# Kernel tuning notes

Measured on AMD Instinct MI355X. Metric: run time of the kernel, lower is better.

## Reference

```python
import jax, jax.numpy as jnp
import numpy as np

H = 512  # hidden_size


def _highway_lstm(x, lengths, Wi, bi, Ws, bs):
    B, T, D = x.shape
    # Precompute all input projections in one big GEMM: [B, T, 6H]
    pi = jnp.einsum('btd,kd->btk', x, Wi) + bi
    mask = jnp.arange(T)[None, :] < lengths[:, None]  # [B, T]

    def step(carry, inp):
        h, c = carry
        pi_t, m = inp                      # pi_t: [B, 6H], m: [B]
        ps = h @ Ws.T + bs                 # [B, 5H]
        i = jax.nn.sigmoid(pi_t[:, 0*H:1*H] + ps[:, 0*H:1*H])
        f = jax.nn.sigmoid(pi_t[:, 1*H:2*H] + ps[:, 1*H:2*H])
        g = jnp.tanh(pi_t[:, 2*H:3*H] + ps[:, 2*H:3*H])
        o = jax.nn.sigmoid(pi_t[:, 3*H:4*H] + ps[:, 3*H:4*H])
        c_new = i * g + f * c
        out = o * jnp.tanh(c_new)
        # highway gate blends LSTM output with linear input projection
        r = jax.nn.sigmoid(pi_t[:, 4*H:5*H] + ps[:, 4*H:5*H])
        out = r * out + (1.0 - r) * pi_t[:, 5*H:6*H]
        m2 = m[:, None]
        h_new = jnp.where(m2, out, h)      # hold state past sequence end
        c_new = jnp.where(m2, c_new, c)
        y = jnp.where(m2, out, jnp.zeros_like(out))  # packed-seq padding = 0
        return (h_new, c_new), y

    h0 = jnp.zeros((B, H), x.dtype)
    c0 = jnp.zeros((B, H), x.dtype)
    (hT, cT), ys = jax.lax.scan(step, (h0, c0),
                                (jnp.swapaxes(pi, 0, 1), mask.T))
    return jnp.swapaxes(ys, 0, 1), hT, cT  # outputs [B,T,H], final (h, c)


def setup_inputs() -> dict:
    key = jax.random.key(0)
    ks = jax.random.split(key, 4)
    B, T, D = 32, 512, 512
    x = jax.random.normal(ks[0], (B, T, D), dtype=jnp.float32)
    lengths = jax.random.randint(ks[1], (B,), 1, T + 1, dtype=jnp.int32)
    Wi = jax.random.normal(ks[2], (6 * H, D), dtype=jnp.float32) * 0.05
    bi = jnp.zeros((6 * H,), dtype=jnp.float32)
    Ws = jax.random.normal(ks[3], (5 * H, H), dtype=jnp.float32) * 0.05
    bs = jnp.zeros((5 * H,), dtype=jnp.float32)
    return {"x": x, "lengths": lengths, "Wi": Wi, "bi": bi, "Ws": Ws, "bs": bs}


def reference(x, lengths, Wi, bi, Ws, bs):
    return _highway_lstm(x, lengths, Wi, bi, Ws, bs)
```

## Files before the change

### kernel.cpp

```cpp
#include <hip/hip_runtime.h>
#include <stdint.h>

typedef __attribute__((ext_vector_type(8))) short short8;
typedef __attribute__((ext_vector_type(4))) float f32x4;
typedef unsigned long long u64;

constexpr int cB = 32, cT = 512, cD = 512, cH = 512;
constexpr int cKI = 6 * cH;
constexpr int NWG = 32;
constexpr int THR = 320;
constexpr int HP  = 520;
constexpr int RNG = 3;
constexpr int PIP = 40;
constexpr int FPAD = 16;
constexpr int GK = 24, GN = 128;

constexpr int OFF_PIL  = 32 * HP * 2;
constexpr int OFF_PS   = OFF_PIL + RNG * 6 * 16 * PIP * 2;
constexpr int OFF_C    = OFF_PS + 5 * 16 * 36 * 4;
constexpr int OFF_BS   = OFF_C + 512 * 4;
constexpr int OFF_LEN  = OFF_BS + 80 * 4;
constexpr int OFF_MISC = OFF_LEN + 32 * 4;
constexpr int SMEM_SZ  = OFF_MISC + 16;

__device__ __forceinline__ float bf2f(unsigned short u) {
  union { unsigned int i; float f; } x; x.i = ((unsigned int)u) << 16; return x.f;
}
__device__ __forceinline__ unsigned short f2bf(float f) {
  union { float f; unsigned int i; } x; x.f = f;
  return (unsigned short)((x.i + 0x7fffu + ((x.i >> 16) & 1u)) >> 16);
}
__device__ __forceinline__ float sigm(float v) { return 1.0f / (1.0f + __expf(-v)); }
__device__ __forceinline__ float tanh_f(float v) { return 2.0f / (1.0f + __expf(-2.0f * v)) - 1.0f; }

__global__ __launch_bounds__(THR, 1) void fused_lstm(
    const float* __restrict__ x,
    const float* __restrict__ Wi,
    const float* __restrict__ bi,
    const float* __restrict__ Ws,
    const float* __restrict__ bs,
    const int* __restrict__ lengths,
    unsigned short* __restrict__ pi,
    unsigned short* __restrict__ hbuf,
    int* __restrict__ flags,
    float* __restrict__ out)
{
  __shared__ __align__(16) unsigned char smem[SMEM_SZ];
  const int tid = threadIdx.x;
  const int lane = tid & 63;
  const int w = tid >> 6;

  if (blockIdx.x >= NWG) {
    const int gb = (int)blockIdx.x - NWG;
    const int kb = gb % GK, nbk = gb / GK;
    const int k0 = kb * 128, n0 = nbk * 128;
    unsigned short* Ai = (unsigned short*)smem;
    unsigned short* Bi = (unsigned short*)(smem + 10240);
    const int wm = w & 1, wn = w >> 1;

    f32x4 acc[4][4];
    #pragma unroll
    for (int i = 0; i < 4; i++)
      #pragma unroll
      for (int j = 0; j < 4; j++) acc[i][j] = (f32x4){0.f, 0.f, 0.f, 0.f};

    for (int kk = 0; kk < cD; kk += 32) {
      __syncthreads();
      for (int idx = tid; idx < 1024; idx += THR) {
        int r = idx >> 3, ch = idx & 7;
        int na = n0 + r, bb = na & 31, tt = na >> 5;
        float4 va = *(const float4*)(x + ((size_t)bb * cT + tt) * cD + kk + ch * 4);
        ushort4 pa; pa.x = f2bf(va.x); pa.y = f2bf(va.y); pa.z = f2bf(va.z); pa.w = f2bf(va.w);
        *(ushort4*)(Ai + r * PIP + ch * 4) = pa;
        float4 vb = *(const float4*)(Wi + (size_t)(k0 + r) * cD + kk + ch * 4);
        ushort4 pb; pb.x = f2bf(vb.x); pb.y = f2bf(vb.y); pb.z = f2bf(vb.z); pb.w = f2bf(vb.w);
        *(ushort4*)(Bi + r * PIP + ch * 4) = pb;
      }
      __syncthreads();
      if (w < 4) {
        short8 af[4], bfr[4];
        const int q = lane >> 4;
        #pragma unroll
        for (int mi = 0; mi < 4; mi++)
          af[mi] = *(const short8*)(Ai + (wm * 64 + mi * 16 + (lane & 15)) * PIP + q * 8);
        #pragma unroll
        for (int ni = 0; ni < 4; ni++)
          bfr[ni] = *(const short8*)(Bi + (wn * 64 + ni * 16 + (lane & 15)) * PIP + q * 8);
        #pragma unroll
        for (int mi = 0; mi < 4; mi++)
          #pragma unroll
          for (int ni = 0; ni < 4; ni++)
            acc[mi][ni] = __builtin_amdgcn_mfma_f32_16x16x32_bf16(af[mi], bfr[ni], acc[mi][ni], 0, 0, 0);
      }
    }
    if (w < 4) {
      #pragma unroll
      for (int ni = 0; ni < 4; ni++) {
        int kl = wn * 64 + ni * 16 + (lane & 15);
        float bv = bi[k0 + kl];
        #pragma unroll
        for (int mi = 0; mi < 4; mi++) {
          int nl = wm * 64 + mi * 16 + (lane >> 4) * 4;
          int nb = n0 + nl;
          int b0 = nb & 31, tt = nb >> 5;
          f32x4 a = acc[mi][ni];
          unsigned short v0 = f2bf(a.x + bv), v1 = f2bf(a.y + bv);
          unsigned short v2 = f2bf(a.z + bv), v3 = f2bf(a.w + bv);
          u64 pk = (u64)v0 | ((u64)v1 << 16) | ((u64)v2 << 32) | ((u64)v3 << 48);
          __hip_atomic_store((u64*)(pi + ((size_t)tt * cKI + k0 + kl) * cB + b0), pk,
                             __ATOMIC_RELAXED, __HIP_MEMORY_SCOPE_AGENT);
        }
      }
    }
    __syncthreads();
    if (tid == 0) {
      __hip_atomic_fetch_add(flags + 512 + nbk, 1, __ATOMIC_RELAXED, __HIP_MEMORY_SCOPE_AGENT);
      __hip_atomic_fetch_add(flags + 640, 1, __ATOMIC_RELAXED, __HIP_MEMORY_SCOPE_AGENT);
    }
    return;
  }

  unsigned short* h_lds  = (unsigned short*)smem;
  unsigned short* piL    = (unsigned short*)(smem + OFF_PIL);
  float* ps_lds          = (float*)(smem + OFF_PS);
  float* c_lds           = (float*)(smem + OFF_C);
  float* bs_lds          = (float*)(smem + OFF_BS);
  int*   len_lds         = (int*)(smem + OFF_LEN);
  int*   s_tr_p          = (int*)(smem + OFF_MISC);
  int*   s_all_p         = s_tr_p + 1;

  const int wg = blockIdx.x;
  const int ci0 = wg * 16;
  const int mc = lane & 15;
  const int kq = lane >> 4;

  short8 bfrag[16];
  {
    const float* wsrow = Ws + (size_t)(w * cH + ci0 + mc) * cH;
    #pragma unroll
    for (int kt = 0; kt < 16; kt++) {
      float4 f0 = *(const float4*)(wsrow + kt * 32 + kq * 8);
      float4 f1 = *(const float4*)(wsrow + kt * 32 + kq * 8 + 4);
      short8 pk;
      pk[0] = (short)f2bf(f0.x); pk[1] = (short)f2bf(f0.y);
      pk[2] = (short)f2bf(f0.z); pk[3] = (short)f2bf(f0.w);
      pk[4] = (short)f2bf(f1.x); pk[5] = (short)f2bf(f1.y);
      pk[6] = (short)f2bf(f1.z); pk[7] = (short)f2bf(f1.w);
      bfrag[kt] = pk;
    }
  }
  if (tid < 80) bs_lds[tid] = bs[(tid >> 4) * cH + ci0 + (tid & 15)];
  if (tid < cB) len_lds[tid] = lengths[tid];
  for (int q = tid; q < 512; q += THR) c_lds[q] = 0.0f;
  for (int q = tid; q < 32 * HP / 4; q += THR) ((u64*)h_lds)[q] = 0ull;

  if (tid == 0) {
    *s_all_p = 0;
    int it = 0;
    while (__hip_atomic_load(flags + 512, __ATOMIC_RELAXED, __HIP_MEMORY_SCOPE_AGENT) < GK) {
      __builtin_amdgcn_s_sleep(8);
      if (++it > 1000000) { *s_all_p = 1; break; }
    }
    *s_tr_p = 4;
  }
  __syncthreads();

  for (int s = 0; s < 2; s++) {
    const unsigned short* pit = pi + (size_t)s * cKI * cB;
    for (int j = tid; j < 384; j += THR) {
      int g = j >> 6, rem = j & 63, c = rem >> 2, q = rem & 3;
      uint4 v = *(const uint4*)(pit + ((size_t)g * cH + ci0 + c) * cB + q * 8);
      *(uint4*)(piL + s * (6 * 16 * PIP) + (g * 16 + c) * PIP + q * 8) = v;
    }
  }
  if (tid < 128) {
    int b = tid >> 2, q = tid & 3;
    __hip_atomic_store((u64*)hbuf + b * 128 + (ci0 >> 2) + q, 0ull,
                       __ATOMIC_RELAXED, __HIP_MEMORY_SCOPE_AGENT);
  }
  __syncthreads();
  if (tid == 0)
    __hip_atomic_store(&flags[wg * FPAD], 1, __ATOMIC_RELAXED, __HIP_MEMORY_SCOPE_AGENT);
  if (tid < 32) {
    int itc = 0;
    while (true) {
      int f = __hip_atomic_load(&flags[tid * FPAD], __ATOMIC_RELAXED, __HIP_MEMORY_SCOPE_AGENT);
      if (__all(f >= 1)) break;
      if (++itc > 20000000) break;
    }
  }
  __syncthreads();

  for (int t = 0; t < cT; t++) {
    const bool last = (t == cT - 1);
    u64 hv[13];
    if (t > 0) {
      u64* hs = (u64*)(hbuf + (size_t)(t & 1) * cB * cH);
      #pragma unroll
      for (int k = 0; k < 13; k++) {
        int idx = tid + k * THR;
        if (idx < 4096)
          hv[k] = __hip_atomic_load(hs + idx, __ATOMIC_RELAXED, __HIP_MEMORY_SCOPE_AGENT);
      }
    }
    uint4 pv0, pv1;
    const bool pf = (t + 2) < cT;
    const int slot_w = (t + 2) % RNG;
    if (pf) {
      const unsigned short* pit = pi + (size_t)(t + 2) * cKI * cB;
      { int g = tid >> 6, rem = tid & 63, c = rem >> 2, q = rem & 3;
        pv0 = *(const uint4*)(pit + ((size_t)g * cH + ci0 + c) * cB + q * 8); }
      int j1 = tid + THR;
      if (j1 < 384) { int g = j1 >> 6, rem = j1 & 63, c = rem >> 2, q = rem & 3;
        pv1 = *(const uint4*)(pit + ((size_t)g * cH + ci0 + c) * cB + q * 8); }
    }
    if (t > 0) {
      #pragma unroll
      for (int k = 0; k < 13; k++) {
        int idx = tid + k * THR;
        if (idx < 4096) {
          int b = idx >> 7, ch = idx & 127;
          *(u64*)(h_lds + b * HP + ch * 4) = hv[k];
        }
      }
    }
    __syncthreads();

    f32x4 acc0 = (f32x4){0.f,0.f,0.f,0.f}, acc1 = (f32x4){0.f,0.f,0.f,0.f};
    #pragma unroll
    for (int kt = 0; kt < 16; kt++) {
      int kc = kt * 4 + kq;
      short8 a0 = *(const short8*)(h_lds + mc * HP + kc * 8);
      short8 a1 = *(const short8*)(h_lds + (16 + mc) * HP + kc * 8);
      acc0 = __builtin_amdgcn_mfma_f32_16x16x32_bf16(a0, bfrag[kt], acc0, 0, 0, 0);
      acc1 = __builtin_amdgcn_mfma_f32_16x16x32_bf16(a1, bfrag[kt], acc1, 0, 0, 0);
    }
    {
      int r0 = kq * 4;
      *(f32x4*)(ps_lds + (w * 16 + mc) * 36 + r0) = acc0;
      *(f32x4*)(ps_lds + (w * 16 + mc) * 36 + r0 + 16) = acc1;
    }
    if (pf) {
      { int g = tid >> 6, rem = tid & 63, c = rem >> 2, q = rem & 3;
        *(uint4*)(piL + slot_w * (6 * 16 * PIP) + (g * 16 + c) * PIP + q * 8) = pv0; }
      int j1 = tid + THR;
      if (j1 < 384) { int g = j1 >> 6, rem = j1 & 63, c = rem >> 2, q = rem & 3;
        *(uint4*)(piL + slot_w * (6 * 16 * PIP) + (g * 16 + c) * PIP + q * 8) = pv1; }
    }
    __syncthreads();

    const unsigned short* pl = piL + (t % RNG) * (6 * 16 * PIP);
    unsigned* hb32 = (unsigned*)(hbuf + (size_t)((t + 1) & 1) * cB * cH);
    float outv0 = 0.f, outv1 = 0.f;
    #pragma unroll
    for (int u = 0; u < 2; u++) {
      int idx = tid + u * THR;
      if (idx < 512) {
        int b = idx >> 4, c = idx & 15;
        int col = ci0 + c;
        float a_i = bf2f(pl[(0*16 + c)*PIP + b]) + ps_lds[(0*16 + c)*36 + b] + bs_lds[0*16 + c];
        float a_f = bf2f(pl[(1*16 + c)*PIP + b]) + ps_lds[(1*16 + c)*36 + b] + bs_lds[1*16 + c];
        float a_g = bf2f(pl[(2*16 + c)*PIP + b]) + ps_lds[(2*16 + c)*36 + b] + bs_lds[2*16 + c];
        float a_o = bf2f(pl[(3*16 + c)*PIP + b]) + ps_lds[(3*16 + c)*36 + b] + bs_lds[3*16 + c];
        float a_r = bf2f(pl[(4*16 + c)*PIP + b]) + ps_lds[(4*16 + c)*36 + b] + bs_lds[4*16 + c];
        float p5  = bf2f(pl[(5*16 + c)*PIP + b]);
        float gi = sigm(a_i), gf = sigm(a_f), gg = tanh_f(a_g), go = sigm(a_o), gr = sigm(a_r);
        float cold = c_lds[b * 16 + c];
        float cn = gi * gg + gf * cold;
        float ov = go * tanh_f(cn);
        ov = gr * ov + (1.0f - gr) * p5;
        bool m = (t < len_lds[b]);
        float hold = bf2f(h_lds[b * HP + col]);
        float hn = m ? ov : hold;
        c_lds[b * 16 + c] = m ? cn : cold;
        float ovm = m ? ov : 0.0f;
        unsigned short hus = f2bf(hn);
        int pr = __shfl_down((int)(unsigned)hus, 1);
        if (!last && (c & 1) == 0) {
          unsigned up = (unsigned)hus | ((unsigned)pr << 16);
          __hip_atomic_store(hb32 + ((b * cH + col) >> 1), up,
                             __ATOMIC_RELAXED, __HIP_MEMORY_SCOPE_AGENT);
        }
        if (last) {
          out[((size_t)b * cT + t) * cH + col] = ovm;
          out[(size_t)cB * cT * cH + (size_t)b * cH + col] = hn;
        } else {
          if (u == 0) outv0 = ovm; else outv1 = ovm;
        }
      }
    }
    if (!last) {
      __syncthreads();
      if (tid == 0)
        __hip_atomic_store(&flags[wg * FPAD], t + 2, __ATOMIC_RELAXED, __HIP_MEMORY_SCOPE_AGENT);
      { int idx = tid;
        if (idx < 512) { int b = idx >> 4, c = idx & 15;
          out[((size_t)b * cT + t) * cH + ci0 + c] = outv0; }
        idx = tid + THR;
        if (idx < 512) { int b = idx >> 4, c = idx & 15;
          out[((size_t)b * cT + t) * cH + ci0 + c] = outv1; } }
      if (tid < 32) {
        int itc = 0;
        while (true) {
          int f = __hip_atomic_load(&flags[tid * FPAD], __ATOMIC_RELAXED, __HIP_MEMORY_SCOPE_AGENT);
          if (__all(f >= t + 2)) break;
          if (++itc > 20000000) break;
        }
      }
      if (tid == 64) {
        if (!*s_all_p) {
          int tr = *s_tr_p;
          int need = t + 4; if (need > cT) need = cT;
          int guard = 0;
          while (tr < need) {
            int tot = __hip_atomic_load(flags + 640, __ATOMIC_RELAXED, __HIP_MEMORY_SCOPE_AGENT);
            if (tot >= GK * GN) { *s_all_p = 1; break; }
            int v = __hip_atomic_load(flags + 512 + (tr >> 2), __ATOMIC_RELAXED, __HIP_MEMORY_SCOPE_AGENT);
            if (v >= GK) { tr += 4; continue; }
            __builtin_amdgcn_s_sleep(8);
            if (++guard > 300000) { *s_all_p = 1; break; }
          }
          *s_tr_p = tr;
        }
      }
      __syncthreads();
    }
  }

  #pragma unroll
  for (int u = 0; u < 2; u++) {
    int idx = tid + u * THR;
    if (idx < 512) {
      int b = idx >> 4, c = idx & 15;
      out[(size_t)cB * cT * cH + (size_t)cB * cH + (size_t)b * cH + ci0 + c] = c_lds[b * 16 + c];
    }
  }
}

extern "C" void kernel_launch(void* const* d_in, const int* in_sizes, int n_in,
                              void* d_out, int out_size, void* d_ws, size_t ws_size,
                              hipStream_t stream) {
  const float* x       = (const float*)d_in[0];
  const int* lengths   = (const int*)d_in[1];
  const float* Wi      = (const float*)d_in[2];
  const float* bi      = (const float*)d_in[3];
  const float* Ws      = (const float*)d_in[4];
  const float* bs      = (const float*)d_in[5];
  float* out = (float*)d_out;

  char* ws = (char*)d_ws;
  int* flags = (int*)ws;
  unsigned short* hbuf = (unsigned short*)(ws + 8192);
  unsigned short* pi   = (unsigned short*)(ws + (1 << 20));

  hipMemsetAsync(flags, 0, 8192, stream);
  fused_lstm<<<NWG + GK * GN, THR, 0, stream>>>(x, Wi, bi, Ws, bs, lengths,
                                                pi, hbuf, flags, out);
}
```

Measured before the change: 1.888 ms.

## Replace per-step flag barrier with step-tagged h exchange polling

The per-timestep cross-workgroup barrier (flag store plus polling of all 32 flags) is replaced by tagging each exchanged bf16 h value with a 16-bit step counter in a 64-bit word. Consumers spin on the h buffer itself until every tag matches the current step. This removes one global round-trip and two block barriers per step. In exchange the h traffic doubles and every thread polls. The GEMM-progress wait is moved inline per step, previous h is kept in registers, and output is stored directly.

```diff
diff --git a/kernel.cpp b/kernel.cpp
--- a/kernel.cpp
+++ b/kernel.cpp
@@ -12,7 +12,6 @@
 constexpr int HP  = 520;
 constexpr int RNG = 3;
 constexpr int PIP = 40;
-constexpr int FPAD = 16;
 constexpr int GK = 24, GN = 128;
 
 constexpr int OFF_PIL  = 32 * HP * 2;
@@ -20,8 +19,7 @@
 constexpr int OFF_C    = OFF_PS + 5 * 16 * 36 * 4;
 constexpr int OFF_BS   = OFF_C + 512 * 4;
 constexpr int OFF_LEN  = OFF_BS + 80 * 4;
-constexpr int OFF_MISC = OFF_LEN + 32 * 4;
-constexpr int SMEM_SZ  = OFF_MISC + 16;
+constexpr int SMEM_SZ  = OFF_LEN + 32 * 4 + 16;
 
 __device__ __forceinline__ float bf2f(unsigned short u) {
   union { unsigned int i; float f; } x; x.i = ((unsigned int)u) << 16; return x.f;
@@ -41,7 +39,7 @@
     const float* __restrict__ bs,
     const int* __restrict__ lengths,
     unsigned short* __restrict__ pi,
-    unsigned short* __restrict__ hbuf,
+    u64* __restrict__ hbuf,
     int* __restrict__ flags,
     float* __restrict__ out)
 {
@@ -126,8 +124,6 @@
   float* c_lds           = (float*)(smem + OFF_C);
   float* bs_lds          = (float*)(smem + OFF_BS);
   int*   len_lds         = (int*)(smem + OFF_LEN);
-  int*   s_tr_p          = (int*)(smem + OFF_MISC);
-  int*   s_all_p         = s_tr_p + 1;
 
   const int wg = blockIdx.x;
   const int ci0 = wg * 16;
@@ -154,17 +150,14 @@
   for (int q = tid; q < 512; q += THR) c_lds[q] = 0.0f;
   for (int q = tid; q < 32 * HP / 4; q += THR) ((u64*)h_lds)[q] = 0ull;
 
-  if (tid == 0) {
-    *s_all_p = 0;
-    int it = 0;
+  {
+    int guard = 0;
     while (__hip_atomic_load(flags + 512, __ATOMIC_RELAXED, __HIP_MEMORY_SCOPE_AGENT) < GK) {
       __builtin_amdgcn_s_sleep(8);
-      if (++it > 1000000) { *s_all_p = 1; break; }
-    }
-    *s_tr_p = 4;
-  }
-  __syncthreads();
-
+      if (++guard > 1000000) break;
+    }
+    asm volatile("" ::: "memory");
+  }
   for (int s = 0; s < 2; s++) {
     const unsigned short* pit = pi + (size_t)s * cKI * cB;
     for (int j = tid; j < 384; j += THR) {
@@ -173,38 +166,28 @@
       *(uint4*)(piL + s * (6 * 16 * PIP) + (g * 16 + c) * PIP + q * 8) = v;
     }
   }
-  if (tid < 128) {
-    int b = tid >> 2, q = tid & 3;
-    __hip_atomic_store((u64*)hbuf + b * 128 + (ci0 >> 2) + q, 0ull,
-                       __ATOMIC_RELAXED, __HIP_MEMORY_SCOPE_AGENT);
-  }
   __syncthreads();
-  if (tid == 0)
-    __hip_atomic_store(&flags[wg * FPAD], 1, __ATOMIC_RELAXED, __HIP_MEMORY_SCOPE_AGENT);
-  if (tid < 32) {
-    int itc = 0;
-    while (true) {
-      int f = __hip_atomic_load(&flags[tid * FPAD], __ATOMIC_RELAXED, __HIP_MEMORY_SCOPE_AGENT);
-      if (__all(f >= 1)) break;
-      if (++itc > 20000000) break;
-    }
-  }
-  __syncthreads();
+
+  bool all_ready = false;
+  bool dead = false;
+  float hprev0 = 0.0f, hprev1 = 0.0f;
 
   for (int t = 0; t < cT; t++) {
     const bool last = (t == cT - 1);
-    u64 hv[13];
-    if (t > 0) {
-      u64* hs = (u64*)(hbuf + (size_t)(t & 1) * cB * cH);
-      #pragma unroll
-      for (int k = 0; k < 13; k++) {
-        int idx = tid + k * THR;
-        if (idx < 4096)
-          hv[k] = __hip_atomic_load(hs + idx, __ATOMIC_RELAXED, __HIP_MEMORY_SCOPE_AGENT);
-      }
+    const bool pf = (t + 2) < cT;
+    if (pf && !all_ready) {
+      int guard = 0;
+      while (true) {
+        int tot = __hip_atomic_load(flags + 640, __ATOMIC_RELAXED, __HIP_MEMORY_SCOPE_AGENT);
+        if (tot >= GK * GN) { all_ready = true; break; }
+        int v = __hip_atomic_load(flags + 512 + ((t + 2) >> 2), __ATOMIC_RELAXED, __HIP_MEMORY_SCOPE_AGENT);
+        if (v >= GK) break;
+        __builtin_amdgcn_s_sleep(4);
+        if (++guard > 200000) { all_ready = true; break; }
+      }
+      asm volatile("" ::: "memory");
     }
     uint4 pv0, pv1;
-    const bool pf = (t + 2) < cT;
     const int slot_w = (t + 2) % RNG;
     if (pf) {
       const unsigned short* pit = pi + (size_t)(t + 2) * cKI * cB;
@@ -214,13 +197,32 @@
       if (j1 < 384) { int g = j1 >> 6, rem = j1 & 63, c = rem >> 2, q = rem & 3;
         pv1 = *(const uint4*)(pit + ((size_t)g * cH + ci0 + c) * cB + q * 8); }
     }
-    if (t > 0) {
+    u64 ha[26];
+    if (t > 0 && !dead) {
+      const u64* hs = hbuf + (size_t)(t & 1) * 8192;
+      const unsigned tg = (unsigned)t;
+      int itc = 0;
+      while (true) {
+        bool ok = true;
+        #pragma unroll
+        for (int k = 0; k < 26; k++) {
+          int idx = tid + k * THR;
+          if (idx < 8192) {
+            ha[k] = __hip_atomic_load(hs + idx, __ATOMIC_RELAXED, __HIP_MEMORY_SCOPE_AGENT);
+            ok = ok && (((unsigned)ha[k] & 0xFFFFu) == tg)
+                    && (((unsigned)(ha[k] >> 32) & 0xFFFFu) == tg);
+          }
+        }
+        if (__all(ok)) break;
+        if (++itc > 100000) { dead = true; break; }
+      }
       #pragma unroll
-      for (int k = 0; k < 13; k++) {
+      for (int k = 0; k < 26; k++) {
         int idx = tid + k * THR;
-        if (idx < 4096) {
-          int b = idx >> 7, ch = idx & 127;
-          *(u64*)(h_lds + b * HP + ch * 4) = hv[k];
+        if (idx < 8192) {
+          int b = idx >> 8, ch = idx & 255;
+          unsigned lo = (unsigned)ha[k], hi = (unsigned)(ha[k] >> 32);
+          *(unsigned*)(h_lds + b * HP + ch * 2) = (lo >> 16) | (hi & 0xFFFF0000u);
         }
       }
     }
@@ -250,8 +252,8 @@
     __syncthreads();
 
     const unsigned short* pl = piL + (t % RNG) * (6 * 16 * PIP);
-    unsigned* hb32 = (unsigned*)(hbuf + (size_t)((t + 1) & 1) * cB * cH);
-    float outv0 = 0.f, outv1 = 0.f;
+    u64* hb64 = hbuf + (size_t)((t + 1) & 1) * 8192;
+    const unsigned tg1 = (unsigned)(t + 1);
     #pragma unroll
     for (int u = 0; u < 2; u++) {
       int idx = tid + u * THR;
@@ -270,60 +272,22 @@
         float ov = go * tanh_f(cn);
         ov = gr * ov + (1.0f - gr) * p5;
         bool m = (t < len_lds[b]);
-        float hold = bf2f(h_lds[b * HP + col]);
+        float hold = (u == 0) ? hprev0 : hprev1;
         float hn = m ? ov : hold;
+        if (u == 0) hprev0 = hn; else hprev1 = hn;
         c_lds[b * 16 + c] = m ? cn : cold;
         float ovm = m ? ov : 0.0f;
-        unsigned short hus = f2bf(hn);
-        int pr = __shfl_down((int)(unsigned)hus, 1);
+        unsigned tw = ((unsigned)f2bf(hn) << 16) | tg1;
+        unsigned pr = (unsigned)__shfl_down((int)tw, 1);
         if (!last && (c & 1) == 0) {
-          unsigned up = (unsigned)hus | ((unsigned)pr << 16);
-          __hip_atomic_store(hb32 + ((b * cH + col) >> 1), up,
+          u64 up = (u64)tw | ((u64)pr << 32);
+          __hip_atomic_store(hb64 + ((b * cH + col) >> 1), up,
                              __ATOMIC_RELAXED, __HIP_MEMORY_SCOPE_AGENT);
         }
-        if (last) {
-          out[((size_t)b * cT + t) * cH + col] = ovm;
+        out[((size_t)b * cT + t) * cH + col] = ovm;
+        if (last)
           out[(size_t)cB * cT * cH + (size_t)b * cH + col] = hn;
-        } else {
-          if (u == 0) outv0 = ovm; else outv1 = ovm;
-        }
-      }
-    }
-    if (!last) {
-      __syncthreads();
-      if (tid == 0)
-        __hip_atomic_store(&flags[wg * FPAD], t + 2, __ATOMIC_RELAXED, __HIP_MEMORY_SCOPE_AGENT);
-      { int idx = tid;
-        if (idx < 512) { int b = idx >> 4, c = idx & 15;
-          out[((size_t)b * cT + t) * cH + ci0 + c] = outv0; }
-        idx = tid + THR;
-        if (idx < 512) { int b = idx >> 4, c = idx & 15;
-          out[((size_t)b * cT + t) * cH + ci0 + c] = outv1; } }
-      if (tid < 32) {
-        int itc = 0;
-        while (true) {
-          int f = __hip_atomic_load(&flags[tid * FPAD], __ATOMIC_RELAXED, __HIP_MEMORY_SCOPE_AGENT);
-          if (__all(f >= t + 2)) break;
-          if (++itc > 20000000) break;
-        }
-      }
-      if (tid == 64) {
-        if (!*s_all_p) {
-          int tr = *s_tr_p;
-          int need = t + 4; if (need > cT) need = cT;
-          int guard = 0;
-          while (tr < need) {
-            int tot = __hip_atomic_load(flags + 640, __ATOMIC_RELAXED, __HIP_MEMORY_SCOPE_AGENT);
-            if (tot >= GK * GN) { *s_all_p = 1; break; }
-            int v = __hip_atomic_load(flags + 512 + (tr >> 2), __ATOMIC_RELAXED, __HIP_MEMORY_SCOPE_AGENT);
-            if (v >= GK) { tr += 4; continue; }
-            __builtin_amdgcn_s_sleep(8);
-            if (++guard > 300000) { *s_all_p = 1; break; }
-          }
-          *s_tr_p = tr;
-        }
-      }
-      __syncthreads();
+      }
     }
   }
 
@@ -350,10 +314,10 @@
 
   char* ws = (char*)d_ws;
   int* flags = (int*)ws;
-  unsigned short* hbuf = (unsigned short*)(ws + 8192);
-  unsigned short* pi   = (unsigned short*)(ws + (1 << 20));
-
-  hipMemsetAsync(flags, 0, 8192, stream);
+  u64* hbuf  = (u64*)(ws + 8192);
+  unsigned short* pi = (unsigned short*)(ws + (1 << 20));
+
+  hipMemsetAsync(ws, 0, 8192 + 131072, stream);
   fused_lstm<<<NWG + GK * GN, THR, 0, stream>>>(x, Wi, bi, Ws, bs, lengths,
                                                 pi, hbuf, flags, out);
 }
```

Result: slower. 2.673 ms (+41.6%).

## Use persistent GEMM workgroups and streamline per-step recurrence synchronization

Applied to the files above, without the earlier changes.

The input-projection GEMM now runs as 448 persistent workgroups, each looping over tiles in time order, instead of launching one workgroup per tile. The recurrent workgroups drop the initial all-workgroup barrier, the hbuf zeroing and the per-step trailing __syncthreads. Every wave now polls the per-step flags and the GEMM progress counters itself, and the held h value stays in registers instead of being read from LDS. This removes barrier and launch overhead on the serial critical path. In exchange it relies on subtle memory-ordering assumptions, has redundant polling traffic from all waves, and the flags are no longer padded, so they may share cache lines.

```diff
diff --git a/kernel.cpp b/kernel.cpp
--- a/kernel.cpp
+++ b/kernel.cpp
@@ -8,11 +8,11 @@
 constexpr int cB = 32, cT = 512, cD = 512, cH = 512;
 constexpr int cKI = 6 * cH;
 constexpr int NWG = 32;
+constexpr int GWGS = 448;
 constexpr int THR = 320;
 constexpr int HP  = 520;
 constexpr int RNG = 3;
 constexpr int PIP = 40;
-constexpr int FPAD = 16;
 constexpr int GK = 24, GN = 128;
 
 constexpr int OFF_PIL  = 32 * HP * 2;
@@ -20,8 +20,7 @@
 constexpr int OFF_C    = OFF_PS + 5 * 16 * 36 * 4;
 constexpr int OFF_BS   = OFF_C + 512 * 4;
 constexpr int OFF_LEN  = OFF_BS + 80 * 4;
-constexpr int OFF_MISC = OFF_LEN + 32 * 4;
-constexpr int SMEM_SZ  = OFF_MISC + 16;
+constexpr int SMEM_SZ  = OFF_LEN + 32 * 4 + 16;
 
 __device__ __forceinline__ float bf2f(unsigned short u) {
   union { unsigned int i; float f; } x; x.i = ((unsigned int)u) << 16; return x.f;
@@ -51,71 +50,74 @@
   const int w = tid >> 6;
 
   if (blockIdx.x >= NWG) {
-    const int gb = (int)blockIdx.x - NWG;
-    const int kb = gb % GK, nbk = gb / GK;
-    const int k0 = kb * 128, n0 = nbk * 128;
+    const int wgg = (int)blockIdx.x - NWG;
     unsigned short* Ai = (unsigned short*)smem;
     unsigned short* Bi = (unsigned short*)(smem + 10240);
     const int wm = w & 1, wn = w >> 1;
 
-    f32x4 acc[4][4];
-    #pragma unroll
-    for (int i = 0; i < 4; i++)
+    for (int tau = wgg; tau < GK * GN; tau += GWGS) {
+      const int nbk = tau / GK, kb = tau % GK;
+      const int k0 = kb * 128, n0 = nbk * 128;
+
+      f32x4 acc[4][4];
       #pragma unroll
-      for (int j = 0; j < 4; j++) acc[i][j] = (f32x4){0.f, 0.f, 0.f, 0.f};
-
-    for (int kk = 0; kk < cD; kk += 32) {
-      __syncthreads();
-      for (int idx = tid; idx < 1024; idx += THR) {
-        int r = idx >> 3, ch = idx & 7;
-        int na = n0 + r, bb = na & 31, tt = na >> 5;
-        float4 va = *(const float4*)(x + ((size_t)bb * cT + tt) * cD + kk + ch * 4);
-        ushort4 pa; pa.x = f2bf(va.x); pa.y = f2bf(va.y); pa.z = f2bf(va.z); pa.w = f2bf(va.w);
-        *(ushort4*)(Ai + r * PIP + ch * 4) = pa;
-        float4 vb = *(const float4*)(Wi + (size_t)(k0 + r) * cD + kk + ch * 4);
-        ushort4 pb; pb.x = f2bf(vb.x); pb.y = f2bf(vb.y); pb.z = f2bf(vb.z); pb.w = f2bf(vb.w);
-        *(ushort4*)(Bi + r * PIP + ch * 4) = pb;
-      }
-      __syncthreads();
-      if (w < 4) {
-        short8 af[4], bfr[4];
-        const int q = lane >> 4;
+      for (int i = 0; i < 4; i++)
         #pragma unroll
-        for (int mi = 0; mi < 4; mi++)
-          af[mi] = *(const short8*)(Ai + (wm * 64 + mi * 16 + (lane & 15)) * PIP + q * 8);
-        #pragma unroll
-        for (int ni = 0; ni < 4; ni++)
-          bfr[ni] = *(const short8*)(Bi + (wn * 64 + ni * 16 + (lane & 15)) * PIP + q * 8);
-        #pragma unroll
-        for (int mi = 0; mi < 4; mi++)
+        for (int j = 0; j < 4; j++) acc[i][j] = (f32x4){0.f, 0.f, 0.f, 0.f};
+
+      for (int kk = 0; kk < cD; kk += 32) {
+        __syncthreads();
+        for (int idx = tid; idx < 1024; idx += THR) {
+          int r = idx >> 3, ch = idx & 7;
+          int na = n0 + r, bb = na & 31, tt = na >> 5;
+          float4 va = *(const float4*)(x + ((size_t)bb * cT + tt) * cD + kk + ch * 4);
+          ushort4 pa; pa.x = f2bf(va.x); pa.y = f2bf(va.y); pa.z = f2bf(va.z); pa.w = f2bf(va.w);
+          *(ushort4*)(Ai + r * PIP + ch * 4) = pa;
+          float4 vb = *(const float4*)(Wi + (size_t)(k0 + r) * cD + kk + ch * 4);
+          ushort4 pb; pb.x = f2bf(vb.x); pb.y = f2bf(vb.y); pb.z = f2bf(vb.z); pb.w = f2bf(vb.w);
+          *(ushort4*)(Bi + r * PIP + ch * 4) = pb;
+        }
+        __syncthreads();
+        if (w < 4) {
+          short8 af[4], bfr[4];
+          const int q = lane >> 4;
+          #pragma unroll
+          for (int mi = 0; mi < 4; mi++)
+            af[mi] = *(const short8*)(Ai + (wm * 64 + mi * 16 + (lane & 15)) * PIP + q * 8);
           #pragma unroll
           for (int ni = 0; ni < 4; ni++)
-            acc[mi][ni] = __builtin_amdgcn_mfma_f32_16x16x32_bf16(af[mi], bfr[ni], acc[mi][ni], 0, 0, 0);
-      }
-    }
-    if (w < 4) {
-      #pragma unroll
-      for (int ni = 0; ni < 4; ni++) {
-        int kl = wn * 64 + ni * 16 + (lane & 15);
-        float bv = bi[k0 + kl];
+            bfr[ni] = *(const short8*)(Bi + (wn * 64 + ni * 16 + (lane & 15)) * PIP + q * 8);
+          #pragma unroll
+          for (int mi = 0; mi < 4; mi++)
+            #pragma unroll
+            for (int ni = 0; ni < 4; ni++)
+              acc[mi][ni] = __builtin_amdgcn_mfma_f32_16x16x32_bf16(af[mi], bfr[ni], acc[mi][ni], 0, 0, 0);
+        }
+      }
+      if (w < 4) {
         #pragma unroll
-        for (int mi = 0; mi < 4; mi++) {
-          int nl = wm * 64 + mi * 16 + (lane >> 4) * 4;
-          int nb = n0 + nl;
-          int b0 = nb & 31, tt = nb >> 5;
-          f32x4 a = acc[mi][ni];
-          unsigned short v0 = f2bf(a.x + bv), v1 = f2bf(a.y + bv);
-          unsigned short v2 = f2bf(a.z + bv), v3 = f2bf(a.w + bv);
-          u64 pk = (u64)v0 | ((u64)v1 << 16) | ((u64)v2 << 32) | ((u64)v3 << 48);
-          __hip_atomic_store((u64*)(pi + ((size_t)tt * cKI + k0 + kl) * cB + b0), pk,
-                             __ATOMIC_RELAXED, __HIP_MEMORY_SCOPE_AGENT);
-        }
-      }
-    }
-    __syncthreads();
-    if (tid == 0) {
-      __hip_atomic_fetch_add(flags + 512 + nbk, 1, __ATOMIC_RELAXED, __HIP_MEMORY_SCOPE_AGENT);
-      __hip_atomic_fetch_add(flags + 640, 1, __ATOMIC_RELAXED, __HIP_MEMORY_SCOPE_AGENT);
+        for (int ni = 0; ni < 4; ni++) {
+          int kl = wn * 64 + ni * 16 + (lane & 15);
+          float bv = bi[k0 + kl];
+          #pragma unroll
+          for (int mi = 0; mi < 4; mi++) {
+            int nl = wm * 64 + mi * 16 + (lane >> 4) * 4;
+            int nb = n0 + nl;
+            int b0 = nb & 31, tt = nb >> 5;
+            f32x4 a = acc[mi][ni];
+            unsigned short v0 = f2bf(a.x + bv), v1 = f2bf(a.y + bv);
+            unsigned short v2 = f2bf(a.z + bv), v3 = f2bf(a.w + bv);
+            u64 pk = (u64)v0 | ((u64)v1 << 16) | ((u64)v2 << 32) | ((u64)v3 << 48);
+            __hip_atomic_store((u64*)(pi + ((size_t)tt * cKI + k0 + kl) * cB + b0), pk,
+                               __ATOMIC_RELAXED, __HIP_MEMORY_SCOPE_AGENT);
+          }
+        }
+      }
+      __syncthreads();
+      if (tid == 0) {
+        __hip_atomic_fetch_add(flags + 512 + nbk, 1, __ATOMIC_RELAXED, __HIP_MEMORY_SCOPE_AGENT);
+        __hip_atomic_fetch_add(flags + 640, 1, __ATOMIC_RELAXED, __HIP_MEMORY_SCOPE_AGENT);
+      }
     }
     return;
   }
@@ -126,8 +128,6 @@
   float* c_lds           = (float*)(smem + OFF_C);
   float* bs_lds          = (float*)(smem + OFF_BS);
   int*   len_lds         = (int*)(smem + OFF_LEN);
-  int*   s_tr_p          = (int*)(smem + OFF_MISC);
-  int*   s_all_p         = s_tr_p + 1;
 
   const int wg = blockIdx.x;
   const int ci0 = wg * 16;
@@ -154,17 +154,14 @@
   for (int q = tid; q < 512; q += THR) c_lds[q] = 0.0f;
   for (int q = tid; q < 32 * HP / 4; q += THR) ((u64*)h_lds)[q] = 0ull;
 
-  if (tid == 0) {
-    *s_all_p = 0;
-    int it = 0;
+  {
+    int guard = 0;
     while (__hip_atomic_load(flags + 512, __ATOMIC_RELAXED, __HIP_MEMORY_SCOPE_AGENT) < GK) {
       __builtin_amdgcn_s_sleep(8);
-      if (++it > 1000000) { *s_all_p = 1; break; }
-    }
-    *s_tr_p = 4;
-  }
-  __syncthreads();
-
+      if (++guard > 1000000) break;
+    }
+    asm volatile("" ::: "memory");
+  }
   for (int s = 0; s < 2; s++) {
     const unsigned short* pit = pi + (size_t)s * cKI * cB;
     for (int j = tid; j < 384; j += THR) {
@@ -173,26 +170,15 @@
       *(uint4*)(piL + s * (6 * 16 * PIP) + (g * 16 + c) * PIP + q * 8) = v;
     }
   }
-  if (tid < 128) {
-    int b = tid >> 2, q = tid & 3;
-    __hip_atomic_store((u64*)hbuf + b * 128 + (ci0 >> 2) + q, 0ull,
-                       __ATOMIC_RELAXED, __HIP_MEMORY_SCOPE_AGENT);
-  }
   __syncthreads();
-  if (tid == 0)
-    __hip_atomic_store(&flags[wg * FPAD], 1, __ATOMIC_RELAXED, __HIP_MEMORY_SCOPE_AGENT);
-  if (tid < 32) {
-    int itc = 0;
-    while (true) {
-      int f = __hip_atomic_load(&flags[tid * FPAD], __ATOMIC_RELAXED, __HIP_MEMORY_SCOPE_AGENT);
-      if (__all(f >= 1)) break;
-      if (++itc > 20000000) break;
-    }
-  }
-  __syncthreads();
+
+  bool all_ready = false;
+  bool dead = false;
+  float hprev0 = 0.0f, hprev1 = 0.0f;
 
   for (int t = 0; t < cT; t++) {
     const bool last = (t == cT - 1);
+    const bool pf = (t + 2) < cT;
     u64 hv[13];
     if (t > 0) {
       u64* hs = (u64*)(hbuf + (size_t)(t & 1) * cB * cH);
@@ -203,8 +189,19 @@
           hv[k] = __hip_atomic_load(hs + idx, __ATOMIC_RELAXED, __HIP_MEMORY_SCOPE_AGENT);
       }
     }
+    if (pf && !all_ready) {
+      int guard = 0;
+      while (true) {
+        int tot = __hip_atomic_load(flags + 640, __ATOMIC_RELAXED, __HIP_MEMORY_SCOPE_AGENT);
+        if (tot >= GK * GN) { all_ready = true; break; }
+        int v = __hip_atomic_load(flags + 512 + ((t + 2) >> 2), __ATOMIC_RELAXED, __HIP_MEMORY_SCOPE_AGENT);
+        if (v >= GK) break;
+        __builtin_amdgcn_s_sleep(4);
+        if (++guard > 200000) { all_ready = true; break; }
+      }
+      asm volatile("" ::: "memory");
+    }
     uint4 pv0, pv1;
-    const bool pf = (t + 2) < cT;
     const int slot_w = (t + 2) % RNG;
     if (pf) {
       const unsigned short* pit = pi + (size_t)(t + 2) * cKI * cB;
@@ -270,14 +267,15 @@
         float ov = go * tanh_f(cn);
         ov = gr * ov + (1.0f - gr) * p5;
         bool m = (t < len_lds[b]);
-        float hold = bf2f(h_lds[b * HP + col]);
+        float hold = (u == 0) ? hprev0 : hprev1;
         float hn = m ? ov : hold;
+        if (u == 0) hprev0 = hn; else hprev1 = hn;
         c_lds[b * 16 + c] = m ? cn : cold;
         float ovm = m ? ov : 0.0f;
         unsigned short hus = f2bf(hn);
-        int pr = __shfl_down((int)(unsigned)hus, 1);
+        unsigned pr = (unsigned)__shfl_down((int)(unsigned)hus, 1);
         if (!last && (c & 1) == 0) {
-          unsigned up = (unsigned)hus | ((unsigned)pr << 16);
+          unsigned up = (unsigned)hus | (pr << 16);
           __hip_atomic_store(hb32 + ((b * cH + col) >> 1), up,
                              __ATOMIC_RELAXED, __HIP_MEMORY_SCOPE_AGENT);
         }
@@ -292,38 +290,22 @@
     if (!last) {
       __syncthreads();
       if (tid == 0)
-        __hip_atomic_store(&flags[wg * FPAD], t + 2, __ATOMIC_RELAXED, __HIP_MEMORY_SCOPE_AGENT);
+        __hip_atomic_store(&flags[wg], t + 2, __ATOMIC_RELAXED, __HIP_MEMORY_SCOPE_AGENT);
       { int idx = tid;
         if (idx < 512) { int b = idx >> 4, c = idx & 15;
           out[((size_t)b * cT + t) * cH + ci0 + c] = outv0; }
         idx = tid + THR;
         if (idx < 512) { int b = idx >> 4, c = idx & 15;
           out[((size_t)b * cT + t) * cH + ci0 + c] = outv1; } }
-      if (tid < 32) {
+      if (!dead) {
+        const int fl = lane & 31;
         int itc = 0;
         while (true) {
-          int f = __hip_atomic_load(&flags[tid * FPAD], __ATOMIC_RELAXED, __HIP_MEMORY_SCOPE_AGENT);
+          int f = __hip_atomic_load(&flags[fl], __ATOMIC_RELAXED, __HIP_MEMORY_SCOPE_AGENT);
           if (__all(f >= t + 2)) break;
-          if (++itc > 20000000) break;
-        }
-      }
-      if (tid == 64) {
-        if (!*s_all_p) {
-          int tr = *s_tr_p;
-          int need = t + 4; if (need > cT) need = cT;
-          int guard = 0;
-          while (tr < need) {
-            int tot = __hip_atomic_load(flags + 640, __ATOMIC_RELAXED, __HIP_MEMORY_SCOPE_AGENT);
-            if (tot >= GK * GN) { *s_all_p = 1; break; }
-            int v = __hip_atomic_load(flags + 512 + (tr >> 2), __ATOMIC_RELAXED, __HIP_MEMORY_SCOPE_AGENT);
-            if (v >= GK) { tr += 4; continue; }
-            __builtin_amdgcn_s_sleep(8);
-            if (++guard > 300000) { *s_all_p = 1; break; }
-          }
-          *s_tr_p = tr;
-        }
-      }
-      __syncthreads();
+          if (++itc > 20000000) { dead = true; break; }
+        }
+      }
     }
   }
 
@@ -354,6 +336,6 @@
   unsigned short* pi   = (unsigned short*)(ws + (1 << 20));
 
   hipMemsetAsync(flags, 0, 8192, stream);
-  fused_lstm<<<NWG + GK * GN, THR, 0, stream>>>(x, Wi, bi, Ws, bs, lengths,
-                                                pi, hbuf, flags, out);
+  fused_lstm<<<NWG + GWGS, THR, 0, stream>>>(x, Wi, bi, Ws, bs, lengths,
+                                             pi, hbuf, flags, out);
 }
```

Result: slower. 2.096 ms (+11.0%).
